# Optimization experiments

Hardware: AMD Instinct MI355X
Metric: run time of the kernel (lower is better)

Reference implementation:

```python
import jax, jax.numpy as jnp
import numpy as np

D_MODEL = 4096
N_HEAD = 32
N_KV_HEAD = 8
D_HEAD = D_MODEL // N_HEAD  # 128
B, T = 2, 2048


def setup_inputs() -> dict:
    key = jax.random.key(0)
    ks = jax.random.split(key, 6)
    x = jax.random.normal(ks[0], (B, T, D_MODEL), dtype=jnp.float32)
    # RoPE angles: theta_i = 10000^(-2i/d_head), angle = pos * theta_i
    inv_freq = 1.0 / (10000.0 ** (jnp.arange(0, D_HEAD, 2, dtype=jnp.float32) / D_HEAD))
    angles = jnp.arange(T, dtype=jnp.float32)[:, None] * inv_freq[None, :]  # [T, D_HEAD//2]
    freqs_cos = jnp.cos(angles)
    freqs_sin = jnp.sin(angles)
    s = 0.02
    wq = jax.random.normal(ks[1], (D_MODEL, N_HEAD * D_HEAD), dtype=jnp.float32) * s
    wk = jax.random.normal(ks[2], (D_MODEL, N_KV_HEAD * D_HEAD), dtype=jnp.float32) * s
    wv = jax.random.normal(ks[3], (D_MODEL, N_KV_HEAD * D_HEAD), dtype=jnp.float32) * s
    wo = jax.random.normal(ks[4], (D_MODEL, D_MODEL), dtype=jnp.float32) * s
    return {"x": x, "freqs_cos": freqs_cos, "freqs_sin": freqs_sin,
            "wq": wq, "wk": wk, "wv": wv, "wo": wo}


def _apply_rope(xq, xk, cos, sin):
    # xq: [B,T,Hq,D], xk: [B,T,Hk,D]; cos/sin: [T, D//2]
    def rot(t):
        tr = t.astype(jnp.float32).reshape(*t.shape[:-1], -1, 2)  # [B,T,H,D//2,2]
        xr, xi = tr[..., 0], tr[..., 1]
        c = cos[None, :, None, :]
        s = sin[None, :, None, :]
        out_r = xr * c - xi * s
        out_i = xr * s + xi * c
        return jnp.stack([out_r, out_i], axis=-1).reshape(t.shape).astype(t.dtype)
    return rot(xq), rot(xk)


def reference(x, freqs_cos, freqs_sin, wq, wk, wv, wo):
    Bq, Tq, _ = x.shape
    xq = (x @ wq).reshape(Bq, Tq, N_HEAD, D_HEAD)
    xk = (x @ wk).reshape(Bq, Tq, N_KV_HEAD, D_HEAD)
    xv = (x @ wv).reshape(Bq, Tq, N_KV_HEAD, D_HEAD)
    xq, xk = _apply_rope(xq, xk, freqs_cos, freqs_sin)
    # [B,H,T,D]
    xq = xq.transpose(0, 2, 1, 3)
    xk = xk.transpose(0, 2, 1, 3)
    xv = xv.transpose(0, 2, 1, 3)
    # GQA: repeat kv heads
    rep = N_HEAD // N_KV_HEAD
    xk = jnp.repeat(xk, rep, axis=1)
    xv = jnp.repeat(xv, rep, axis=1)
    scale = 1.0 / np.sqrt(D_HEAD)
    scores = jnp.einsum("bhqd,bhkd->bhqk", xq, xk) * scale
    causal = jnp.tril(jnp.ones((Tq, Tq), dtype=bool))
    scores = jnp.where(causal[None, None], scores, jnp.finfo(scores.dtype).min)
    probs = jax.nn.softmax(scores, axis=-1)
    z = jnp.einsum("bhqk,bhkd->bhqd", probs, xv)
    z = z.transpose(0, 2, 1, 3).reshape(Bq, Tq, D_MODEL)
    return z @ wo
```

## Files before the change

### kernel.cpp

```cpp
#include <hip/hip_runtime.h>

typedef unsigned short u16;
typedef unsigned int u32;
typedef u16 u16x8 __attribute__((ext_vector_type(8)));
typedef __bf16 bf16x8 __attribute__((ext_vector_type(8)));
typedef float f32x4 __attribute__((ext_vector_type(4)));

#define TOKENS 4096
#define DMODEL 4096
#define QKVN 6144
#define NHEAD 32
#define NKV 8
#define DHEAD 128
#define SEQ 2048

#define BARRIER() asm volatile("s_barrier" ::: "memory")
#define LGKM0() asm volatile("s_waitcnt lgkmcnt(0)" ::: "memory")
#define VMCNT(n) asm volatile("s_waitcnt vmcnt(" #n ")" ::: "memory")

__device__ inline u16 f2bf(float f) {
    unsigned int u = __float_as_uint(f);
    u += 0x7fffu + ((u >> 16) & 1u);
    return (u16)(u >> 16);
}
__device__ inline float bf2f(u16 h) {
    return __uint_as_float(((unsigned int)h) << 16);
}
__device__ inline u32 pack2bf(float a, float b) {
    return (u32)f2bf(a) | ((u32)f2bf(b) << 16);
}
__device__ inline f32x4 mfma16(bf16x8 a, bf16x8 b, f32x4 c) {
    return __builtin_amdgcn_mfma_f32_16x16x32_bf16(a, b, c, 0, 0, 0);
}
__device__ __forceinline__ void gload16(const u16* g, u16* l) {
    __builtin_amdgcn_global_load_lds((const __attribute__((address_space(1))) u32*)g,
                                     (__attribute__((address_space(3))) u32*)l, 16, 0, 0);
}

__global__ __launch_bounds__(256) void f2bf_kernel(const float* __restrict__ in,
                                                   u16* __restrict__ out, int n) {
    int i = (blockIdx.x * 256 + threadIdx.x) * 4;
    if (i >= n) return;
    float4 v = *(const float4*)(in + i);
    u16 o0 = f2bf(v.x), o1 = f2bf(v.y), o2 = f2bf(v.z), o3 = f2bf(v.w);
    u16* p = out + i;
    p[0] = o0; p[1] = o1; p[2] = o2; p[3] = o3;
}

__global__ __launch_bounds__(256) void transpose_kernel(const float* __restrict__ in,
                                                        u16* __restrict__ out,
                                                        int K, int N) {
    __shared__ float t[32][33];
    int n0 = blockIdx.x * 32, k0 = blockIdx.y * 32;
    int x = threadIdx.x, y = threadIdx.y;
#pragma unroll
    for (int i = 0; i < 4; i++)
        t[y + 8 * i][x] = in[(size_t)(k0 + y + 8 * i) * N + n0 + x];
    __syncthreads();
#pragma unroll
    for (int i = 0; i < 4; i++)
        out[(size_t)(n0 + y + 8 * i) * K + k0 + x] = f2bf(t[x][y + 8 * i]);
}

__global__ __launch_bounds__(256) void vtrans_kernel(const u16* __restrict__ qkv,
                                                     u16* __restrict__ vt) {
    __shared__ u16 t[32][33];
    int b = blockIdx.z;
    int c0 = blockIdx.x * 32;
    int r0 = blockIdx.y * 32;
    int x = threadIdx.x, y = threadIdx.y;
    const u16* in = qkv + (size_t)(b * SEQ) * QKVN + 5120;
#pragma unroll
    for (int i = 0; i < 4; i++)
        t[y + 8 * i][x] = in[(size_t)(r0 + y + 8 * i) * QKVN + c0 + x];
    __syncthreads();
    u16* out = vt + (size_t)b * 1024 * SEQ;
#pragma unroll
    for (int i = 0; i < 4; i++)
        out[(size_t)(c0 + y + 8 * i) * SEQ + r0 + x] = t[x][y + 8 * i];
}

template <bool OUT_F32>
__global__ __launch_bounds__(512, 2) void gemm256(const u16* __restrict__ A,
                                                  const u16* __restrict__ Bt,
                                                  void* __restrict__ C,
                                                  int M, int N, int K) {
    __shared__ u16 lds[2][2][2][128 * 64];
    const int tid = threadIdx.x, wave = tid >> 6, lane = tid & 63;
    const int quad = lane >> 4, l16 = lane & 15;
    const int wave_m = wave >> 2, wave_n = wave & 3;
    const int m0 = blockIdx.y * 256, n0 = blockIdx.x * 256;
    const int wn = wave_n * 64;
    const int nk = K >> 6;

    const int srow = wave * 16 + (lane >> 3);
    const int scol = ((lane & 7) ^ (lane >> 3)) << 3;
    const u16* ga0 = A + (size_t)(m0 + srow) * K + scol;
    const u16* gb0 = Bt + (size_t)(n0 + srow) * K + scol;

    auto STAGE = [&](int op, int buf, int half, int kt) {
        const u16* src = (op ? gb0 : ga0) + (size_t)(half * 128) * K + (kt << 6);
        u16* dst = &lds[op][buf][half][wave * 1024];
        gload16(src, dst);
        gload16(src + (size_t)8 * K, dst + 512);
    };
    auto FRAG = [&](const u16* base, int lr, int c) -> bf16x8 {
        int idx = (lr * 64 + c) ^ ((lr & 7) << 3);
        return *(const bf16x8*)(base + idx);
    };

    f32x4 acc[8][4] = {};

    STAGE(1, 0, 0, 0); STAGE(1, 0, 1, 0); STAGE(0, 0, 0, 0); STAGE(0, 0, 1, 0);
    STAGE(1, 1, 0, 1); STAGE(1, 1, 1, 1); STAGE(0, 1, 0, 1);
    VMCNT(6);
    BARRIER();

    bf16x8 af[4][2], bfr[4][2];

    auto KTILE = [&](int kt, int cur) {
        const int nxt = cur ^ 1;
        const int k1 = kt + 1 < nk ? kt + 1 : nk - 1;
        const int k2 = kt + 2 < nk ? kt + 2 : nk - 1;
        const u16* aB = &lds[0][cur][wave_m][0];
#pragma unroll
        for (int i = 0; i < 4; i++)
#pragma unroll
            for (int kk = 0; kk < 2; kk++)
                af[i][kk] = FRAG(aB, i * 16 + l16, kk * 32 + quad * 8);
#pragma unroll
        for (int j = 0; j < 4; j++) {
            const int brow = wn + j * 16;
            const u16* bB = &lds[1][cur][brow >> 7][0];
#pragma unroll
            for (int kk = 0; kk < 2; kk++)
                bfr[j][kk] = FRAG(bB, (brow & 127) + l16, kk * 32 + quad * 8);
        }
        STAGE(0, nxt, 1, k1);
        BARRIER();
        __builtin_amdgcn_s_setprio(1);
#pragma unroll
        for (int i = 0; i < 4; i++)
#pragma unroll
            for (int j = 0; j < 2; j++)
#pragma unroll
                for (int kk = 0; kk < 2; kk++)
                    acc[i][j] = mfma16(af[i][kk], bfr[j][kk], acc[i][j]);
        __builtin_amdgcn_s_setprio(0);
        LGKM0();
        BARRIER();
        STAGE(1, cur, 0, k2);
        BARRIER();
        __builtin_amdgcn_s_setprio(1);
#pragma unroll
        for (int i = 0; i < 4; i++)
#pragma unroll
            for (int j = 0; j < 2; j++)
#pragma unroll
                for (int kk = 0; kk < 2; kk++)
                    acc[i][2 + j] = mfma16(af[i][kk], bfr[2 + j][kk], acc[i][2 + j]);
        __builtin_amdgcn_s_setprio(0);
        BARRIER();
#pragma unroll
        for (int i = 0; i < 4; i++)
#pragma unroll
            for (int kk = 0; kk < 2; kk++)
                af[i][kk] = FRAG(aB, 64 + i * 16 + l16, kk * 32 + quad * 8);
        STAGE(1, cur, 1, k2);
        BARRIER();
        __builtin_amdgcn_s_setprio(1);
#pragma unroll
        for (int i = 0; i < 4; i++)
#pragma unroll
            for (int j = 0; j < 2; j++)
#pragma unroll
                for (int kk = 0; kk < 2; kk++)
                    acc[4 + i][j] = mfma16(af[i][kk], bfr[j][kk], acc[4 + i][j]);
        __builtin_amdgcn_s_setprio(0);
        LGKM0();
        BARRIER();
        STAGE(0, cur, 0, k2);
        BARRIER();
        __builtin_amdgcn_s_setprio(1);
#pragma unroll
        for (int i = 0; i < 4; i++)
#pragma unroll
            for (int j = 0; j < 2; j++)
#pragma unroll
                for (int kk = 0; kk < 2; kk++)
                    acc[4 + i][2 + j] = mfma16(af[i][kk], bfr[2 + j][kk], acc[4 + i][2 + j]);
        __builtin_amdgcn_s_setprio(0);
        VMCNT(6);
        BARRIER();
    };

    for (int kt = 0; kt < nk; kt += 2) {
        KTILE(kt, 0);
        KTILE(kt + 1, 1);
    }

    VMCNT(0);

#pragma unroll
    for (int i = 0; i < 8; i++)
#pragma unroll
        for (int j = 0; j < 4; j++) {
            const int row = m0 + wave_m * 128 + i * 16 + quad * 4;
            const int col = n0 + wn + j * 16 + l16;
            if (OUT_F32) {
                float* Cf = (float*)C;
#pragma unroll
                for (int r = 0; r < 4; r++)
                    Cf[(size_t)(row + r) * N + col] = acc[i][j][r];
            } else {
                u16* Cb = (u16*)C;
#pragma unroll
                for (int r = 0; r < 4; r++)
                    Cb[(size_t)(row + r) * N + col] = f2bf(acc[i][j][r]);
            }
        }
}

__global__ __launch_bounds__(256) void rope2_kernel(u16* __restrict__ buf,
                                                    const float* __restrict__ cosb,
                                                    const float* __restrict__ sinb,
                                                    int nheads, int colbase, float scale) {
    int idx = blockIdx.x * 256 + threadIdx.x;
    int p = idx & 63;
    int rest = idx >> 6;
    int h = rest & (nheads - 1);
    int tok = rest / nheads;
    int tseq = tok & (SEQ - 1);
    float c = cosb[tseq * 64 + p], s = sinb[tseq * 64 + p];
    u32* ptr = (u32*)(buf + (size_t)tok * QKVN + colbase + h * DHEAD + 2 * p);
    u32 v = *ptr;
    float xr = bf2f((u16)(v & 0xffff)), xi = bf2f((u16)(v >> 16));
    float orr = (xr * c - xi * s) * scale;
    float oii = (xr * s + xi * c) * scale;
    *ptr = pack2bf(orr, oii);
}

#define NINF (-__builtin_inff())

__global__ __launch_bounds__(256, 2) void flash2_kernel(const u16* __restrict__ QKV,
                                                        const u16* __restrict__ Vt,
                                                        u16* __restrict__ Z) {
    __shared__ u16 lK[2][4][64 * 32];
    __shared__ u16 lV[2][2][128 * 32];
    __shared__ u16 lP[4][2][32 * 32];
    int tid = threadIdx.x, wave = tid >> 6, lane = tid & 63;
    int quad = lane >> 4, l16 = lane & 15;
    int qt = 15 - (int)blockIdx.x;
    int h = blockIdx.y, b = blockIdx.z;
    int kvh = h >> 2;
    int Q0 = qt * 128;
    int qw = Q0 + wave * 32;
    int lrow = lane >> 2;
    int scol = (((lane & 3) ^ ((lane >> 3) & 3)) << 3);
    const int sw = (l16 >> 1) & 3;
    const int qsw = (quad ^ sw) * 8;

    bf16x8 qf[2][4];
#pragma unroll
    for (int nt = 0; nt < 2; nt++) {
        const u16* qp = QKV + (size_t)(b * SEQ + qw + nt * 16 + l16) * QKVN + h * DHEAD;
#pragma unroll
        for (int kk = 0; kk < 4; kk++)
            qf[nt][kk] = *(const bf16x8*)(qp + kk * 32 + quad * 8);
    }

    f32x4 o[2][8] = {};
    float mrun[2] = {NINF, NINF};
    float lrun[2] = {0.f, 0.f};

    const u16* gk = QKV + (size_t)(b * SEQ + lrow) * QKVN + DMODEL + kvh * DHEAD + wave * 32 + scol;
    int kf_w = wave >> 1, dh_w = (wave & 1) * 64;
    const u16* gv = Vt + ((size_t)(b * NKV + kvh) * DHEAD + dh_w + lrow) * SEQ + kf_w * 32 + scol;

    auto STAGEKV = [&](int kt, int buf) {
        int key0 = kt * 64;
        u16* lk = lK[buf][wave];
        u16* lv = lV[buf][kf_w] + dh_w * 32;
#pragma unroll
        for (int g = 0; g < 4; g++)
            gload16(gk + (size_t)(key0 + g * 16) * QKVN, lk + g * 512);
#pragma unroll
        for (int g = 0; g < 4; g++)
            gload16(gv + (size_t)(g * 16) * SEQ + key0, lv + g * 512);
    };

    int nkt = 2 * qt + 2;
    STAGEKV(0, 0);

    for (int kt = 0; kt < nkt; kt++) {
        int cur = kt & 1;
        int ks = (kt + 1 < nkt) ? kt + 1 : nkt - 1;
        STAGEKV(ks, cur ^ 1);
        VMCNT(8);
        BARRIER();

        int key0 = kt * 64;
        if (key0 <= qw + 31) {
            f32x4 st[4][2] = {};
#pragma unroll
            for (int kk = 0; kk < 4; kk++) {
                bf16x8 kfr[4];
#pragma unroll
                for (int mt = 0; mt < 4; mt++)
                    kfr[mt] = *(const bf16x8*)(lK[cur][kk] + (mt * 16 + l16) * 32 + qsw);
                __builtin_amdgcn_s_setprio(1);
#pragma unroll
                for (int mt = 0; mt < 4; mt++)
#pragma unroll
                    for (int nt = 0; nt < 2; nt++)
                        st[mt][nt] = mfma16(kfr[mt], qf[nt][kk], st[mt][nt]);
                __builtin_amdgcn_s_setprio(0);
            }
            if (key0 + 63 > qw) {
#pragma unroll
                for (int mt = 0; mt < 4; mt++)
#pragma unroll
                    for (int nt = 0; nt < 2; nt++)
#pragma unroll
                        for (int r = 0; r < 4; r++)
                            if (key0 + mt * 16 + quad * 4 + r > qw + nt * 16 + l16)
                                st[mt][nt][r] = NINF;
            }
            float alpha[2];
#pragma unroll
            for (int nt = 0; nt < 2; nt++) {
                float vmax = NINF;
#pragma unroll
                for (int mt = 0; mt < 4; mt++)
#pragma unroll
                    for (int r = 0; r < 4; r++) vmax = fmaxf(vmax, st[mt][nt][r]);
                vmax = fmaxf(vmax, __shfl_xor(vmax, 16));
                vmax = fmaxf(vmax, __shfl_xor(vmax, 32));
                float mnew = fmaxf(mrun[nt], vmax);
                alpha[nt] = __expf(mrun[nt] - mnew);
                mrun[nt] = mnew;
                float rsum = 0.f;
#pragma unroll
                for (int mt = 0; mt < 4; mt++)
#pragma unroll
                    for (int r = 0; r < 4; r++) {
                        float p = __expf(st[mt][nt][r] - mnew);
                        st[mt][nt][r] = p;
                        rsum += p;
                    }
                rsum += __shfl_xor(rsum, 16);
                rsum += __shfl_xor(rsum, 32);
                lrun[nt] = lrun[nt] * alpha[nt] + rsum;
#pragma unroll
                for (int mt = 0; mt < 4; mt++) {
                    u32 p01 = pack2bf(st[mt][nt][0], st[mt][nt][1]);
                    u32 p23 = pack2bf(st[mt][nt][2], st[mt][nt][3]);
                    uint2 pk; pk.x = p01; pk.y = p23;
                    int gphys = ((((mt & 1) * 2) + (quad >> 1)) ^ sw) * 8 + (quad & 1) * 4;
                    *(uint2*)(lP[wave][mt >> 1] + (nt * 16 + l16) * 32 + gphys) = pk;
                }
            }
#pragma unroll
            for (int mtq = 0; mtq < 2; mtq++)
#pragma unroll
                for (int r = 0; r < 4; r++) {
                    float av = __shfl(alpha[mtq], quad * 4 + r);
#pragma unroll
                    for (int ntd = 0; ntd < 8; ntd++) o[mtq][ntd][r] *= av;
                }
#pragma unroll
            for (int kfi = 0; kfi < 2; kfi++) {
                bf16x8 pf0 = *(const bf16x8*)(lP[wave][kfi] + l16 * 32 + qsw);
                bf16x8 pf1 = *(const bf16x8*)(lP[wave][kfi] + (16 + l16) * 32 + qsw);
                __builtin_amdgcn_s_setprio(1);
#pragma unroll
                for (int ntd = 0; ntd < 8; ntd++) {
                    bf16x8 vfr = *(const bf16x8*)(lV[cur][kfi] + (ntd * 16 + l16) * 32 + qsw);
                    o[0][ntd] = mfma16(pf0, vfr, o[0][ntd]);
                    o[1][ntd] = mfma16(pf1, vfr, o[1][ntd]);
                }
                __builtin_amdgcn_s_setprio(0);
            }
        }
        LGKM0();
        BARRIER();
    }
    VMCNT(0);

#pragma unroll
    for (int mtq = 0; mtq < 2; mtq++) {
        float linv[4];
#pragma unroll
        for (int r = 0; r < 4; r++) linv[r] = 1.0f / __shfl(lrun[mtq], quad * 4 + r);
#pragma unroll
        for (int ntd = 0; ntd < 8; ntd++)
#pragma unroll
            for (int r = 0; r < 4; r++) {
                int q = qw + mtq * 16 + quad * 4 + r;
                Z[(size_t)(b * SEQ + q) * DMODEL + h * DHEAD + ntd * 16 + l16] =
                    f2bf(o[mtq][ntd][r] * linv[r]);
            }
    }
}

extern "C" void kernel_launch(void* const* d_in, const int* in_sizes, int n_in,
                              void* d_out, int out_size, void* d_ws, size_t ws_size,
                              hipStream_t stream) {
    const float* x    = (const float*)d_in[0];
    const float* fcos = (const float*)d_in[1];
    const float* fsin = (const float*)d_in[2];
    const float* wq   = (const float*)d_in[3];
    const float* wk   = (const float*)d_in[4];
    const float* wv   = (const float*)d_in[5];
    const float* wo   = (const float*)d_in[6];
    float* out = (float*)d_out;
    char* ws = (char*)d_ws;

    const size_t MiB = 1024ull * 1024ull;
    u16* xb    = (u16*)(ws);
    u16* zb    = xb;
    u16* wqkvt = (u16*)(ws + 32 * MiB);
    u16* wot   = (u16*)(ws + 80 * MiB);
    u16* qkv   = (u16*)(ws + 112 * MiB);
    u16* vtb   = (u16*)(ws + 160 * MiB);

    f2bf_kernel<<<16384, 256, 0, stream>>>(x, xb, TOKENS * DMODEL);
    dim3 tb(32, 8);
    transpose_kernel<<<dim3(128, 128), tb, 0, stream>>>(wq, wqkvt, 4096, 4096);
    transpose_kernel<<<dim3(32, 128), tb, 0, stream>>>(wk, wqkvt + (size_t)4096 * 4096, 4096, 1024);
    transpose_kernel<<<dim3(32, 128), tb, 0, stream>>>(wv, wqkvt + (size_t)5120 * 4096, 4096, 1024);
    transpose_kernel<<<dim3(128, 128), tb, 0, stream>>>(wo, wot, 4096, 4096);

    gemm256<false><<<dim3(24, 16), 512, 0, stream>>>(xb, wqkvt, qkv, 4096, QKVN, 4096);

    rope2_kernel<<<32768, 256, 0, stream>>>(qkv, fcos, fsin, NHEAD, 0, 0.08838834764831845f);
    rope2_kernel<<<8192, 256, 0, stream>>>(qkv, fcos, fsin, NKV, DMODEL, 1.0f);

    vtrans_kernel<<<dim3(32, 64, 2), tb, 0, stream>>>(qkv, vtb);

    flash2_kernel<<<dim3(16, 32, 2), 256, 0, stream>>>(qkv, vtb, zb);

    gemm256<true><<<dim3(16, 16), 512, 0, stream>>>(zb, wot, out, 4096, 4096, 4096);
}
```

Before: 772.5 us.

## Load V fragments directly from global, remap blocks for L2 reuse, use exp2

The flash attention kernel stops staging V through shared memory. Each wave loads its V MFMA fragments straight from global memory into registers, and K staging now waits on vmcnt(0) before the barrier. Blocks are launched on a 1D grid and remapped so that the heads sharing a KV head and batch run close together, which should improve L2 reuse of K/V. The softmax now uses a native exp2 with log2(e) folded into the Q scale, cutting a multiply per exponential, at the cost of more register pressure and a less deep prefetch pipeline.

After: 808.7 us. +4.7%, slower.

```diff
diff --git a/kernel.cpp b/kernel.cpp
--- a/kernel.cpp
+++ b/kernel.cpp
@@ -35,6 +35,13 @@
 __device__ __forceinline__ void gload16(const u16* g, u16* l) {
     __builtin_amdgcn_global_load_lds((const __attribute__((address_space(1))) u32*)g,
                                      (__attribute__((address_space(3))) u32*)l, 16, 0, 0);
+}
+__device__ __forceinline__ float fexp2(float x) {
+#if __has_builtin(__builtin_amdgcn_exp2f)
+    return __builtin_amdgcn_exp2f(x);
+#else
+    return __expf(x * 0.69314718056f);
+#endif
 }
 
 __global__ __launch_bounds__(256) void f2bf_kernel(const float* __restrict__ in,
@@ -246,13 +253,14 @@
                                                         const u16* __restrict__ Vt,
                                                         u16* __restrict__ Z) {
     __shared__ u16 lK[2][4][64 * 32];
-    __shared__ u16 lV[2][2][128 * 32];
     __shared__ u16 lP[4][2][32 * 32];
     int tid = threadIdx.x, wave = tid >> 6, lane = tid & 63;
     int quad = lane >> 4, l16 = lane & 15;
-    int qt = 15 - (int)blockIdx.x;
-    int h = blockIdx.y, b = blockIdx.z;
-    int kvh = h >> 2;
+    int bi = blockIdx.x;
+    int dd = (bi & 7) * 128 + (bi >> 3);
+    int b = dd >> 9, kvh = (dd >> 6) & 7, hh = (dd >> 4) & 3;
+    int qt = 15 - (dd & 15);
+    int h = kvh * 4 + hh;
     int Q0 = qt * 128;
     int qw = Q0 + wave * 32;
     int lrow = lane >> 2;
@@ -274,33 +282,36 @@
     float lrun[2] = {0.f, 0.f};
 
     const u16* gk = QKV + (size_t)(b * SEQ + lrow) * QKVN + DMODEL + kvh * DHEAD + wave * 32 + scol;
-    int kf_w = wave >> 1, dh_w = (wave & 1) * 64;
-    const u16* gv = Vt + ((size_t)(b * NKV + kvh) * DHEAD + dh_w + lrow) * SEQ + kf_w * 32 + scol;
-
-    auto STAGEKV = [&](int kt, int buf) {
+    const u16* gvb = Vt + ((size_t)(b * NKV + kvh) * DHEAD + l16) * SEQ + quad * 8;
+
+    auto STAGEK = [&](int kt, int buf) {
         int key0 = kt * 64;
         u16* lk = lK[buf][wave];
-        u16* lv = lV[buf][kf_w] + dh_w * 32;
 #pragma unroll
         for (int g = 0; g < 4; g++)
             gload16(gk + (size_t)(key0 + g * 16) * QKVN, lk + g * 512);
-#pragma unroll
-        for (int g = 0; g < 4; g++)
-            gload16(gv + (size_t)(g * 16) * SEQ + key0, lv + g * 512);
     };
 
     int nkt = 2 * qt + 2;
-    STAGEKV(0, 0);
+    STAGEK(0, 0);
 
     for (int kt = 0; kt < nkt; kt++) {
         int cur = kt & 1;
+        int key0 = kt * 64;
+        VMCNT(0);
         int ks = (kt + 1 < nkt) ? kt + 1 : nkt - 1;
-        STAGEKV(ks, cur ^ 1);
-        VMCNT(8);
-        BARRIER();
-
-        int key0 = kt * 64;
+        STAGEK(ks, cur ^ 1);
+        BARRIER();
+
         if (key0 <= qw + 31) {
+            bf16x8 vfr[2][8];
+#pragma unroll
+            for (int kfi = 0; kfi < 2; kfi++)
+#pragma unroll
+                for (int ntd = 0; ntd < 8; ntd++)
+                    vfr[kfi][ntd] =
+                        *(const bf16x8*)(gvb + (size_t)(ntd * 16) * SEQ + key0 + kfi * 32);
+
             f32x4 st[4][2] = {};
 #pragma unroll
             for (int kk = 0; kk < 4; kk++) {
@@ -337,14 +348,14 @@
                 vmax = fmaxf(vmax, __shfl_xor(vmax, 16));
                 vmax = fmaxf(vmax, __shfl_xor(vmax, 32));
                 float mnew = fmaxf(mrun[nt], vmax);
-                alpha[nt] = __expf(mrun[nt] - mnew);
+                alpha[nt] = fexp2(mrun[nt] - mnew);
                 mrun[nt] = mnew;
                 float rsum = 0.f;
 #pragma unroll
                 for (int mt = 0; mt < 4; mt++)
 #pragma unroll
                     for (int r = 0; r < 4; r++) {
-                        float p = __expf(st[mt][nt][r] - mnew);
+                        float p = fexp2(st[mt][nt][r] - mnew);
                         st[mt][nt][r] = p;
                         rsum += p;
                     }
@@ -375,9 +386,8 @@
                 __builtin_amdgcn_s_setprio(1);
 #pragma unroll
                 for (int ntd = 0; ntd < 8; ntd++) {
-                    bf16x8 vfr = *(const bf16x8*)(lV[cur][kfi] + (ntd * 16 + l16) * 32 + qsw);
-                    o[0][ntd] = mfma16(pf0, vfr, o[0][ntd]);
-                    o[1][ntd] = mfma16(pf1, vfr, o[1][ntd]);
+                    o[0][ntd] = mfma16(pf0, vfr[kfi][ntd], o[0][ntd]);
+                    o[1][ntd] = mfma16(pf1, vfr[kfi][ntd], o[1][ntd]);
                 }
                 __builtin_amdgcn_s_setprio(0);
             }
@@ -433,12 +443,12 @@
 
     gemm256<false><<<dim3(24, 16), 512, 0, stream>>>(xb, wqkvt, qkv, 4096, QKVN, 4096);
 
-    rope2_kernel<<<32768, 256, 0, stream>>>(qkv, fcos, fsin, NHEAD, 0, 0.08838834764831845f);
+    rope2_kernel<<<32768, 256, 0, stream>>>(qkv, fcos, fsin, NHEAD, 0, 0.12751743f);
     rope2_kernel<<<8192, 256, 0, stream>>>(qkv, fcos, fsin, NKV, DMODEL, 1.0f);
 
     vtrans_kernel<<<dim3(32, 64, 2), tb, 0, stream>>>(qkv, vtb);
 
-    flash2_kernel<<<dim3(16, 32, 2), 256, 0, stream>>>(qkv, vtb, zb);
+    flash2_kernel<<<1024, 256, 0, stream>>>(qkv, vtb, zb);
 
     gemm256<true><<<dim3(16, 16), 512, 0, stream>>>(zb, wot, out, 4096, 4096, 4096);
 }
```
